# Kernel tuning notes

Hardware: AMD Instinct MI355X
Metric: run time of the kernel (lower is better)

## Reference

```python
import jax, jax.numpy as jnp
import numpy as np

B, D_IN, D_Z, D_H, D_T, D_REC = 8192, 1024, 256, 256, 16, 256


def _softplus_beta(x, beta):
    # torch F.softplus(x, beta) = (1/beta) * log(1 + exp(beta*x))
    return jax.nn.softplus(beta * x) / beta


def setup_inputs() -> dict:
    key = jax.random.key(0)
    ks = jax.random.split(key, 17)
    w = lambda k, o, i: jax.random.normal(k, (o, i), jnp.float32) * (1.0 / np.sqrt(i))
    return {
        "I_t": jax.random.uniform(ks[0], (B, D_IN), jnp.float32),
        "h_m_1": jax.random.uniform(ks[1], (B, D_H), jnp.float32),
        "z_m_1": jax.random.uniform(ks[2], (B, D_Z), jnp.float32),
        "theta_m_1": jax.random.normal(ks[3], (B, D_T), jnp.float32),
        "eps_z": jax.random.normal(ks[4], (B, D_Z), jnp.float32),
        "eps_zhat": jax.random.normal(ks[5], (B, D_Z), jnp.float32),
        "W_post_mu": w(ks[6], D_Z, D_IN),
        "W_post_lv": w(ks[7], D_Z, D_IN),
        "W_z2h": w(ks[8], D_H, D_Z),
        "W_h2h": w(ks[9], D_H, D_H),
        "W_prior_mu": w(ks[10], D_Z, D_H),
        "W_prior_lv": w(ks[11], D_Z, D_H),
        "W_i2t": w(ks[12], D_T, D_IN),
        "W_vip2t": w(ks[13], D_T, D_Z),
        "W_t2z": w(ks[14], D_Z, D_T),
        "W_rec1": w(ks[15], D_REC, D_Z),
        "W_rec2": w(ks[16], D_IN, D_REC),
    }


def reference(I_t, h_m_1, z_m_1, theta_m_1, eps_z, eps_zhat,
              W_post_mu, W_post_lv, W_z2h, W_h2h, W_prior_mu, W_prior_lv,
              W_i2t, W_vip2t, W_t2z, W_rec1, W_rec2):
    relu = jax.nn.relu
    # prior pathway (perception_only=True branch)
    mu_p = relu(h_m_1 @ W_prior_mu.T)                       # [B, D_Z]
    sigma_p = _softplus_beta(h_m_1 @ W_prior_lv.T, 1.2)     # [B, D_Z]
    # theta dynamics; vip_to_theta has Positive parametrization -> relu(W)
    theta_h = (0.5 * theta_m_1 + 0.1 * (I_t @ W_i2t.T)
               - jax.lax.stop_gradient(sigma_p) @ relu(W_vip2t).T)  # [B, D_T]
    theta = 0.001 * _softplus_beta(theta_h, 0.5)
    # posterior + reparameterized sample
    mu_q = relu(I_t @ W_post_mu.T)
    sigma_q = relu(I_t @ W_post_lv.T)
    raw_z = jnp.clip(mu_q + eps_z * sigma_q, 0.0, 1.0)
    thresholds = 10.0 * (theta @ relu(W_t2z).T)             # Positive parametrization
    z = relu(raw_z - thresholds)                            # [B, D_Z]
    # reconstruction (two bias-free linears + sigmoid)
    I_hat = jax.nn.sigmoid((z @ W_rec1.T) @ W_rec2.T)       # [B, D_IN]
    # higher-state update and prior sample
    h = relu(z_m_1 @ W_z2h.T + h_m_1 @ W_h2h.T)             # [B, D_H]
    z_hat = mu_p + eps_zhat * sigma_p                       # [B, D_Z]
    # losses (as in torch forward)
    spatial = jnp.mean((I_t - I_hat) ** 2)
    temporal = jnp.mean((jax.lax.stop_gradient(z) - z_hat) ** 2)
    energy = jnp.mean(jnp.abs(z))
    return (I_hat, z, h, z_hat, spatial, temporal, energy)
```

## Files before the change

kernel.cpp:

```cpp
#include <hip/hip_runtime.h>
#include <math.h>

#define BB 8192
#define DIN 1024
#define DZ 256
#define DH 256
#define DT 16
#define DREC 256

#define OFF_IHAT 0
#define OFF_Z    (BB * DIN)
#define OFF_H    (OFF_Z + BB * DZ)
#define OFF_ZHAT (OFF_H + BB * DH)
#define OFF_SCAL (OFF_ZHAT + BB * DZ)

#define WS_HBF   0
#define WS_ZM1   2097152
#define WS_W     4194304
#define W_PM  (WS_W + 0)
#define W_PL  (W_PM + 262144)
#define W_Z2H (W_PL + 262144)
#define W_H2H (W_Z2H + 65536)
#define W_PRM (W_H2H + 65536)
#define W_PRL (W_PRM + 65536)
#define W_I2T (W_PRL + 65536)
#define W_VIP (W_I2T + 16384)
#define W_R1  (W_VIP + 4096)
#define W_R2  (W_R1 + 65536)
#define WS_ENDW  (W_R2 + 262144)
#define WS_SIGMA WS_ENDW
#define WS_ZBF   (WS_SIGMA + 2097152)
#define WS_R1BF  (WS_ZBF + 2097152)

typedef unsigned short u16;
typedef __attribute__((ext_vector_type(8))) unsigned short u16x8;
typedef __attribute__((ext_vector_type(8))) __bf16 bf16x8;
typedef __attribute__((ext_vector_type(4))) float f32x4;

#define MFMA __builtin_amdgcn_mfma_f32_16x16x32_bf16

__device__ inline u16 f2bf(float f) {
  unsigned u = __builtin_bit_cast(unsigned, f);
  u += 0x7fff + ((u >> 16) & 1);
  return (u16)(u >> 16);
}
__device__ inline float softplus_stable(float y) {
  return (y > 20.f) ? y : log1pf(expf(y));
}
__device__ inline bf16x8 gf(const u16* p) {
  return __builtin_bit_cast(bf16x8, *(const u16x8*)p);
}
__device__ inline f32x4 fzero() { return (f32x4){0.f, 0.f, 0.f, 0.f}; }

__device__ inline float block_sum256(float v, float* rbuf) {
#pragma unroll
  for (int off = 32; off > 0; off >>= 1) v += __shfl_down(v, off, 64);
  __syncthreads();
  if ((threadIdx.x & 63) == 0) rbuf[threadIdx.x >> 6] = v;
  __syncthreads();
  return rbuf[0] + rbuf[1] + rbuf[2] + rbuf[3];
}
__device__ inline float block_sum512(float v, float* rbuf) {
#pragma unroll
  for (int off = 32; off > 0; off >>= 1) v += __shfl_down(v, off, 64);
  __syncthreads();
  if ((threadIdx.x & 63) == 0) rbuf[threadIdx.x >> 6] = v;
  __syncthreads();
  float s = 0.f;
#pragma unroll
  for (int i = 0; i < 8; ++i) s += rbuf[i];
  return s;
}

__device__ inline void decode4(int id, int rows, int& row0, int& col0) {
  int xcd = id & 7, t = id >> 3;
  col0 = (t & 3) * 64;
  row0 = ((t >> 2) * 8 + xcd) * rows;
}

__device__ inline void dmaA32(u16* tile, const u16* __restrict__ gsrc,
                              int row0, int ldk, int k0) {
  const int lane = threadIdx.x & 63, w = threadIdx.x >> 6;
  int rb = w * 8;
  int r = rb + (lane >> 3);
  int gl = (lane & 7) ^ (r & 7);
  const u16* src = gsrc + (size_t)(row0 + r) * ldk + k0 + gl * 8;
  u16* dst = tile + rb * 64;
  __builtin_amdgcn_global_load_lds(
      (const __attribute__((address_space(1))) unsigned int*)(const void*)src,
      (__attribute__((address_space(3))) unsigned int*)(void*)dst, 16, 0, 0);
}
__device__ inline void dmaB64(u16* tile, const u16* __restrict__ gsrc,
                              int row0, int ldk, int k0) {
  const int lane = threadIdx.x & 63, w = threadIdx.x >> 6;
#pragma unroll
  for (int c = 0; c < 2; ++c) {
    int rb = w * 16 + c * 8;
    int r = rb + (lane >> 3);
    int gl = (lane & 7) ^ (r & 7);
    const u16* src = gsrc + (size_t)(row0 + r) * ldk + k0 + gl * 8;
    u16* dst = tile + rb * 64;
    __builtin_amdgcn_global_load_lds(
        (const __attribute__((address_space(1))) unsigned int*)(const void*)src,
        (__attribute__((address_space(3))) unsigned int*)(void*)dst, 16, 0, 0);
  }
}
__device__ inline bf16x8 rd(const u16* tile, int r, int gl) {
  return gf(tile + r * 64 + ((gl ^ (r & 7)) * 8));
}

__device__ inline void stg64x128(u16* tile, const u16* __restrict__ g,
                                 int row0, int ldk, int k0) {
  const int lane = threadIdx.x & 63, w = threadIdx.x >> 6;
#pragma unroll
  for (int i = 0; i < 2; ++i) {
    int rb = (w * 2 + i) * 4;
    int r = rb + (lane >> 4);
    int d = lane & 15;
    int s = d ^ (r & 7);
    const u16* src = g + (size_t)(row0 + r) * ldk + k0 + s * 8;
    u16* dst = tile + rb * 128;
    __builtin_amdgcn_global_load_lds(
        (const __attribute__((address_space(1))) unsigned int*)(const void*)src,
        (__attribute__((address_space(3))) unsigned int*)(void*)dst, 16, 0, 0);
  }
}
__device__ inline void stg16x128(u16* tile, const u16* __restrict__ g,
                                 int ldk, int k0) {
  const int lane = threadIdx.x & 63, w = threadIdx.x >> 6;
  if (w < 4) {
    int rb = w * 4;
    int r = rb + (lane >> 4);
    int d = lane & 15;
    int s = d ^ (r & 7);
    const u16* src = g + (size_t)r * ldk + k0 + s * 8;
    u16* dst = tile + rb * 128;
    __builtin_amdgcn_global_load_lds(
        (const __attribute__((address_space(1))) unsigned int*)(const void*)src,
        (__attribute__((address_space(3))) unsigned int*)(void*)dst, 16, 0, 0);
  }
}
__device__ inline bf16x8 rd128(const u16* tile, int r, int j) {
  return gf(tile + r * 128 + ((j ^ (r & 7)) * 8));
}

__device__ inline void lda4(bf16x8 (&ar)[4], const u16* base, int kwin,
                            int fq) {
#pragma unroll
  for (int kk = 0; kk < 4; ++kk) ar[kk] = gf(base + kwin + kk * 32 + fq * 8);
}
__device__ inline void cmpMain(const u16* buf, bf16x8 (&ar)[4], f32x4 (&mu)[4],
                               f32x4 (&sg)[4], f32x4& tt, int frow, int fq) {
#pragma unroll
  for (int kk = 0; kk < 4; ++kk) {
    int j = kk * 4 + fq;
#pragma unroll
    for (int n = 0; n < 4; ++n) {
      mu[n] = MFMA(ar[kk], rd128(buf, n * 16 + frow, j), mu[n], 0, 0, 0);
      sg[n] = MFMA(ar[kk], rd128(buf + 8192, n * 16 + frow, j), sg[n], 0, 0, 0);
    }
    tt = MFMA(ar[kk], rd128(buf + 16384, frow, j), tt, 0, 0, 0);
  }
}
__device__ inline void cmpSig(const u16* buf, bf16x8 (&ar)[4], f32x4& tt,
                              int frow, int fq) {
#pragma unroll
  for (int kk = 0; kk < 4; ++kk)
    tt = MFMA(ar[kk], rd128(buf + 16384, frow, kk * 4 + fq), tt, 0, 0, 0);
}

__global__ __launch_bounds__(256) void k_cvt(
    const float* __restrict__ I_t, const float* __restrict__ h_m_1,
    const float* __restrict__ z_m_1, const float* __restrict__ Wpm,
    const float* __restrict__ Wpl, const float* __restrict__ Wz2h,
    const float* __restrict__ Wh2h, const float* __restrict__ Wprm,
    const float* __restrict__ Wprl, const float* __restrict__ Wi2t,
    const float* __restrict__ Wv, const float* __restrict__ Wr1,
    const float* __restrict__ Wr2, u16* __restrict__ dstI,
    u16* __restrict__ dstW) {
  const int S1 = 8388608, S2 = 10485760, S3 = 12582912, S4 = 12845056,
            S5 = 13107200, S6 = 13172736, S7 = 13238272, S8 = 13303808,
            S9 = 13369344, S10 = 13385728, S11 = 13389824, S12 = 13455360,
            S13 = 13717504;
  int nchunk = S13 / 8;
  for (int c = blockIdx.x * 256 + threadIdx.x; c < nchunk;
       c += gridDim.x * 256) {
    int f = c * 8;
    const float* src;
    float scale = 1.f;
    bool nrelu = false;
    u16* dst;
    if (f < S1) {
      src = I_t + f;
      dst = dstI + f;
    } else {
      dst = dstW + (f - S1);
      if (f < S2)       src = h_m_1 + (f - S1);
      else if (f < S3)  src = z_m_1 + (f - S2);
      else if (f < S4)  src = Wpm + (f - S3);
      else if (f < S5)  src = Wpl + (f - S4);
      else if (f < S6)  src = Wz2h + (f - S5);
      else if (f < S7)  src = Wh2h + (f - S6);
      else if (f < S8)  src = Wprm + (f - S7);
      else if (f < S9)  src = Wprl + (f - S8);
      else if (f < S10) { src = Wi2t + (f - S9);  scale = 0.1f; }
      else if (f < S11) { src = Wv + (f - S10);   nrelu = true; }
      else if (f < S12) src = Wr1 + (f - S11);
      else              src = Wr2 + (f - S12);
    }
    float4 v0 = *(const float4*)(src);
    float4 v1 = *(const float4*)(src + 4);
    float vals[8] = {v0.x, v0.y, v0.z, v0.w, v1.x, v1.y, v1.z, v1.w};
    u16x8 o;
#pragma unroll
    for (int j = 0; j < 8; ++j) {
      float x = vals[j];
      x = nrelu ? -fmaxf(x, 0.f) : x * scale;
      o[j] = f2bf(x);
    }
    *(u16x8*)(dst) = o;
  }
}

__global__ __launch_bounds__(256, 2) void k_hp(
    const u16* __restrict__ h_bf, const u16* __restrict__ zm1,
    const u16* __restrict__ Wh2h, const u16* __restrict__ Wprm,
    const u16* __restrict__ Wprl, const u16* __restrict__ Wz2h,
    const float* __restrict__ eps_zhat, float* __restrict__ h_out,
    float* __restrict__ zhat_out, u16* __restrict__ sigma_bf) {
  __shared__ __align__(16) u16 smem[2 * 14336];
  const int tid = threadIdx.x, lane = tid & 63, w = tid >> 6;
  const int frow = lane & 15, fq = lane >> 4;
  const int wr = w & 1, wc = w >> 1;
  int row0, col0;
  decode4(blockIdx.x, 32, row0, col0);

  f32x4 ah[2], am[2], as_[2];
#pragma unroll
  for (int i = 0; i < 2; ++i) { ah[i] = fzero(); am[i] = fzero(); as_[i] = fzero(); }

  dmaA32(smem, h_bf, row0, DH, 0);
  dmaB64(smem + 2048, Wh2h, col0, DH, 0);
  dmaB64(smem + 6144, Wprm, col0, DH, 0);
  dmaB64(smem + 10240, Wprl, col0, DH, 0);

#pragma unroll 1
  for (int t = 0; t < 8; ++t) {
    __syncthreads();
    u16* cs = smem + (t & 1) * 14336;
    u16* ns = smem + ((t + 1) & 1) * 14336;
    if (t < 7) {
      int u = t + 1;
      if (u < 4) {
        int k0 = u * 64;
        dmaA32(ns, h_bf, row0, DH, k0);
        dmaB64(ns + 2048, Wh2h, col0, DH, k0);
        dmaB64(ns + 6144, Wprm, col0, DH, k0);
        dmaB64(ns + 10240, Wprl, col0, DH, k0);
      } else {
        int k0 = (u - 4) * 64;
        dmaA32(ns, zm1, row0, DZ, k0);
        dmaB64(ns + 2048, Wz2h, col0, DZ, k0);
      }
    }
    const u16* As = cs;
    const u16* B0s = cs + 2048;
    if (t < 4) {
      const u16* B1s = cs + 6144;
      const u16* B2s = cs + 10240;
#pragma unroll
      for (int ks = 0; ks < 2; ++ks) {
        bf16x8 a = rd(As, wr * 16 + frow, ks * 4 + fq);
#pragma unroll
        for (int ni = 0; ni < 2; ++ni) {
          int br = wc * 32 + ni * 16 + frow;
          ah[ni]  = MFMA(a, rd(B0s, br, ks * 4 + fq), ah[ni], 0, 0, 0);
          am[ni]  = MFMA(a, rd(B1s, br, ks * 4 + fq), am[ni], 0, 0, 0);
          as_[ni] = MFMA(a, rd(B2s, br, ks * 4 + fq), as_[ni], 0, 0, 0);
        }
      }
    } else {
#pragma unroll
      for (int ks = 0; ks < 2; ++ks) {
        bf16x8 a = rd(As, wr * 16 + frow, ks * 4 + fq);
#pragma unroll
        for (int ni = 0; ni < 2; ++ni)
          ah[ni] = MFMA(a, rd(B0s, wc * 32 + ni * 16 + frow, ks * 4 + fq),
                        ah[ni], 0, 0, 0);
      }
    }
  }
  __syncthreads();
  float* ht = (float*)smem;
  float* mt = (float*)(smem + 4224);
  float* st = (float*)(smem + 8448);
#pragma unroll
  for (int ni = 0; ni < 2; ++ni)
#pragma unroll
    for (int r = 0; r < 4; ++r) {
      int lr = wr * 16 + fq * 4 + r;
      int ln = wc * 32 + ni * 16 + frow;
      ht[lr * 66 + ln] = fmaxf(ah[ni][r], 0.f);
      mt[lr * 66 + ln] = fmaxf(am[ni][r], 0.f);
      st[lr * 66 + ln] = softplus_stable(1.2f * as_[ni][r]) * (1.f / 1.2f);
    }
  __syncthreads();
  {
    int lr2 = tid >> 3, c0 = (tid & 7) * 8;
    int m2 = row0 + lr2;
    float h8[8], mu8[8], sg8[8];
#pragma unroll
    for (int j = 0; j < 8; ++j) {
      h8[j] = ht[lr2 * 66 + c0 + j];
      mu8[j] = mt[lr2 * 66 + c0 + j];
      sg8[j] = st[lr2 * 66 + c0 + j];
    }
    float* hp = h_out + (size_t)m2 * DH + col0 + c0;
    *(float4*)hp = make_float4(h8[0], h8[1], h8[2], h8[3]);
    *(float4*)(hp + 4) = make_float4(h8[4], h8[5], h8[6], h8[7]);
    const float* ep = eps_zhat + (size_t)m2 * DZ + col0 + c0;
    float4 e0 = ((const float4*)ep)[0], e1 = ((const float4*)ep)[1];
    float e8[8] = {e0.x, e0.y, e0.z, e0.w, e1.x, e1.y, e1.z, e1.w};
    float zh8[8];
    u16x8 sb;
#pragma unroll
    for (int j = 0; j < 8; ++j) {
      zh8[j] = mu8[j] + e8[j] * sg8[j];
      sb[j] = f2bf(sg8[j]);
    }
    float* zp = zhat_out + (size_t)m2 * DZ + col0 + c0;
    *(float4*)zp = make_float4(zh8[0], zh8[1], zh8[2], zh8[3]);
    *(float4*)(zp + 4) = make_float4(zh8[4], zh8[5], zh8[6], zh8[7]);
    *(u16x8*)(sigma_bf + (size_t)m2 * DZ + col0 + c0) = sb;
  }
}

__global__ __launch_bounds__(512, 2) void k_post(
    const u16* __restrict__ I_bf, const u16* __restrict__ Wpm,
    const u16* __restrict__ Wpl, const u16* __restrict__ Wi2t,
    const u16* __restrict__ Wv, const u16* __restrict__ sigma_bf,
    const float* __restrict__ theta_m_1, const float* __restrict__ W_t2z,
    const float* __restrict__ eps_z, const float* __restrict__ zhat,
    float* __restrict__ z_out, u16* __restrict__ z_bf,
    float* __restrict__ scal) {
  __shared__ __align__(16) u16 smem[2 * 18432];
  __shared__ float thwt[128 * 17 + 64 * 17];
  __shared__ float rbuf[8];
  const int tid = threadIdx.x, lane = tid & 63, w = tid >> 6;
  const int frow = lane & 15, fq = lane >> 4;
  int row0, col0;
  {
    int xcd = blockIdx.x & 7, t = blockIdx.x >> 3;
    col0 = (t & 3) * 64;
    row0 = ((t >> 2) * 8 + xcd) * 128;
  }
  u16* b0 = smem;
  u16* b1 = smem + 18432;

  f32x4 mu[4], sg[4], tt = fzero();
#pragma unroll
  for (int i = 0; i < 4; ++i) { mu[i] = fzero(); sg[i] = fzero(); }

  const u16* Abase = I_bf + (size_t)(row0 + w * 16 + frow) * DIN;
  const u16* Sbase = sigma_bf + (size_t)(row0 + w * 16 + frow) * DZ;
  bf16x8 arA[4], arB[4];

#define STGM(buf, k0)                        \
  stg64x128(buf, Wpm, col0, DIN, k0);        \
  stg64x128((buf) + 8192, Wpl, col0, DIN, k0);\
  stg16x128((buf) + 16384, Wi2t, DIN, k0)

  STGM(b0, 0);
  lda4(arA, Abase, 0, fq);
  __syncthreads(); STGM(b1, 128); lda4(arB, Abase, 128, fq);
  cmpMain(b0, arA, mu, sg, tt, frow, fq);
  __syncthreads(); STGM(b0, 256); lda4(arA, Abase, 256, fq);
  cmpMain(b1, arB, mu, sg, tt, frow, fq);
  __syncthreads(); STGM(b1, 384); lda4(arB, Abase, 384, fq);
  cmpMain(b0, arA, mu, sg, tt, frow, fq);
  __syncthreads(); STGM(b0, 512); lda4(arA, Abase, 512, fq);
  cmpMain(b1, arB, mu, sg, tt, frow, fq);
  __syncthreads(); STGM(b1, 640); lda4(arB, Abase, 640, fq);
  cmpMain(b0, arA, mu, sg, tt, frow, fq);
  __syncthreads(); STGM(b0, 768); lda4(arA, Abase, 768, fq);
  cmpMain(b1, arB, mu, sg, tt, frow, fq);
  __syncthreads(); STGM(b1, 896); lda4(arB, Abase, 896, fq);
  cmpMain(b0, arA, mu, sg, tt, frow, fq);
  __syncthreads(); stg16x128(b0 + 16384, Wv, DZ, 0); lda4(arA, Sbase, 0, fq);
  cmpMain(b1, arB, mu, sg, tt, frow, fq);
  __syncthreads(); stg16x128(b1 + 16384, Wv, DZ, 128); lda4(arB, Sbase, 128, fq);
  cmpSig(b0, arA, tt, frow, fq);
  __syncthreads();
  cmpSig(b1, arB, tt, frow, fq);
#undef STGM

  __syncthreads();
  float* mt   = (float*)smem;
  float* st   = (float*)(smem + 16896);
  float* th_s = thwt;
  float* wt_s = thwt + 128 * 17;

#pragma unroll
  for (int r = 0; r < 4; ++r) {
    int lr = w * 16 + fq * 4 + r;
    float th = 0.5f * theta_m_1[(size_t)(row0 + lr) * DT + frow] + tt[r];
    th_s[lr * 17 + frow] = 0.002f * softplus_stable(0.5f * th);
  }
  for (int idx = tid; idx < 64 * 16; idx += 512) {
    int n = idx >> 4, j = idx & 15;
    wt_s[n * 17 + j] = 10.f * fmaxf(W_t2z[(col0 + n) * DT + j], 0.f);
  }
#pragma unroll
  for (int n = 0; n < 4; ++n)
#pragma unroll
    for (int r = 0; r < 4; ++r) {
      int lr = w * 16 + fq * 4 + r;
      int ln = n * 16 + frow;
      mt[lr * 66 + ln] = fmaxf(mu[n][r], 0.f);
      st[lr * 66 + ln] = fmaxf(sg[n][r], 0.f);
    }
  __syncthreads();
  float tsum = 0.f, esum = 0.f;
  {
    int lr2 = tid >> 2, c0 = (tid & 3) * 16;
    int m2 = row0 + lr2;
    float thv[16];
#pragma unroll
    for (int j = 0; j < 16; ++j) thv[j] = th_s[lr2 * 17 + j];
#pragma unroll
    for (int gb = 0; gb < 2; ++gb) {
      int c = c0 + gb * 8;
      float mu8[8], sg8[8];
#pragma unroll
      for (int j = 0; j < 8; ++j) {
        mu8[j] = mt[lr2 * 66 + c + j];
        sg8[j] = st[lr2 * 66 + c + j];
      }
      const float* ep = eps_z + (size_t)m2 * DZ + col0 + c;
      float4 e0 = ((const float4*)ep)[0], e1 = ((const float4*)ep)[1];
      float e8[8] = {e0.x, e0.y, e0.z, e0.w, e1.x, e1.y, e1.z, e1.w};
      float z8[8];
#pragma unroll
      for (int j = 0; j < 8; ++j) {
        float raw = mu8[j] + e8[j] * sg8[j];
        raw = fminf(fmaxf(raw, 0.f), 1.f);
        float thr = 0.f;
#pragma unroll
        for (int jj = 0; jj < 16; ++jj)
          thr = fmaf(thv[jj], wt_s[(c + j) * 17 + jj], thr);
        z8[j] = fmaxf(raw - thr, 0.f);
      }
      float* zp = z_out + (size_t)m2 * DZ + col0 + c;
      *(float4*)zp = make_float4(z8[0], z8[1], z8[2], z8[3]);
      *(float4*)(zp + 4) = make_float4(z8[4], z8[5], z8[6], z8[7]);
      u16x8 zb;
#pragma unroll
      for (int j = 0; j < 8; ++j) zb[j] = f2bf(z8[j]);
      *(u16x8*)(z_bf + (size_t)m2 * DZ + col0 + c) = zb;
      const float* zhp = zhat + (size_t)m2 * DZ + col0 + c;
      float4 h0 = ((const float4*)zhp)[0], h1 = ((const float4*)zhp)[1];
      float zh8[8] = {h0.x, h0.y, h0.z, h0.w, h1.x, h1.y, h1.z, h1.w};
#pragma unroll
      for (int j = 0; j < 8; ++j) {
        float d = z8[j] - zh8[j];
        tsum += d * d;
        esum += z8[j];
      }
    }
  }
  float t = block_sum512(tsum, rbuf);
  if (tid == 0) atomicAdd(scal + 1, t * (1.f / ((float)BB * DZ)));
  float e = block_sum512(esum, rbuf);
  if (tid == 0) atomicAdd(scal + 2, e * (1.f / ((float)BB * DZ)));
}

__global__ __launch_bounds__(256, 4) void k_rec1(const u16* __restrict__ z_bf,
                                                 const u16* __restrict__ Wr1,
                                                 u16* __restrict__ r1_bf) {
  __shared__ __align__(16) u16 smem[2 * 6144];
  const int tid = threadIdx.x, lane = tid & 63, w = tid >> 6;
  const int frow = lane & 15, fq = lane >> 4;
  const int wr = w & 1, wc = w >> 1;
  int row0, col0;
  decode4(blockIdx.x, 32, row0, col0);
  f32x4 acc[2] = {fzero(), fzero()};

  dmaA32(smem, z_bf, row0, DZ, 0);
  dmaB64(smem + 2048, Wr1, col0, DZ, 0);
#pragma unroll 1
  for (int t = 0; t < 4; ++t) {
    __syncthreads();
    u16* cs = smem + (t & 1) * 6144;
    u16* ns = smem + ((t + 1) & 1) * 6144;
    if (t < 3) {
      int k0 = (t + 1) * 64;
      dmaA32(ns, z_bf, row0, DZ, k0);
      dmaB64(ns + 2048, Wr1, col0, DZ, k0);
    }
#pragma unroll
    for (int ks = 0; ks < 2; ++ks) {
      bf16x8 a = rd(cs, wr * 16 + frow, ks * 4 + fq);
#pragma unroll
      for (int ni = 0; ni < 2; ++ni)
        acc[ni] = MFMA(a, rd(cs + 2048, wc * 32 + ni * 16 + frow, ks * 4 + fq),
                       acc[ni], 0, 0, 0);
    }
  }
  __syncthreads();
  float* rt = (float*)smem;
#pragma unroll
  for (int ni = 0; ni < 2; ++ni)
#pragma unroll
    for (int r = 0; r < 4; ++r) {
      int lr = wr * 16 + fq * 4 + r;
      int ln = wc * 32 + ni * 16 + frow;
      rt[lr * 66 + ln] = acc[ni][r];
    }
  __syncthreads();
  {
    int lr2 = tid >> 3, c0 = (tid & 7) * 8;
    int m2 = row0 + lr2;
    u16x8 rb;
#pragma unroll
    for (int j = 0; j < 8; ++j) rb[j] = f2bf(rt[lr2 * 66 + c0 + j]);
    *(u16x8*)(r1_bf + (size_t)m2 * DREC + col0 + c0) = rb;
  }
}

__global__ __launch_bounds__(256, 4) void k_rec2(const u16* __restrict__ r1_bf,
                                                 const u16* __restrict__ Wr2,
                                                 const float* __restrict__ I_t,
                                                 float* __restrict__ ihat_out,
                                                 float* __restrict__ scal) {
  __shared__ __align__(16) u16 smem[2 * 8192];
  __shared__ float rbuf[4];
  const int tid = threadIdx.x, lane = tid & 63, w = tid >> 6;
  const int frow = lane & 15, fq = lane >> 4;
  int row0, col0;
  {
    int id = blockIdx.x;
    int xcd = id & 7, t = id >> 3;
    col0 = (t & 15) * 64;
    row0 = ((t >> 4) * 8 + xcd) * 64;
  }
  f32x4 acc[4] = {fzero(), fzero(), fzero(), fzero()};

  dmaB64(smem, r1_bf, row0, DREC, 0);
  dmaB64(smem + 4096, Wr2, col0, DREC, 0);
#pragma unroll 1
  for (int t = 0; t < 4; ++t) {
    __syncthreads();
    u16* cs = smem + (t & 1) * 8192;
    u16* ns = smem + ((t + 1) & 1) * 8192;
    if (t < 3) {
      int k0 = (t + 1) * 64;
      dmaB64(ns, r1_bf, row0, DREC, k0);
      dmaB64(ns + 4096, Wr2, col0, DREC, k0);
    }
#pragma unroll
    for (int ks = 0; ks < 2; ++ks) {
      bf16x8 a = rd(cs, w * 16 + frow, ks * 4 + fq);
#pragma unroll
      for (int ni = 0; ni < 4; ++ni)
        acc[ni] = MFMA(a, rd(cs + 4096, ni * 16 + frow, ks * 4 + fq),
                       acc[ni], 0, 0, 0);
    }
  }
  float lsum = 0.f;
  float* it = (float*)smem;
#pragma unroll 1
  for (int p = 0; p < 2; ++p) {
    __syncthreads();
    if ((w >> 1) == p) {
#pragma unroll
      for (int ni = 0; ni < 4; ++ni)
#pragma unroll
        for (int r = 0; r < 4; ++r) {
          int lrl = (w & 1) * 16 + fq * 4 + r;
          int ln = ni * 16 + frow;
          it[lrl * 66 + ln] = 1.f / (1.f + expf(-acc[ni][r]));
        }
    }
    __syncthreads();
    int lr2 = tid >> 3, c0 = (tid & 7) * 8;
    int m2 = row0 + p * 32 + lr2;
    float i8[8];
#pragma unroll
    for (int j = 0; j < 8; ++j) i8[j] = it[lr2 * 66 + c0 + j];
    float* op = ihat_out + (size_t)m2 * DIN + col0 + c0;
    *(float4*)op = make_float4(i8[0], i8[1], i8[2], i8[3]);
    *(float4*)(op + 4) = make_float4(i8[4], i8[5], i8[6], i8[7]);
    const float* ip = I_t + (size_t)m2 * DIN + col0 + c0;
    float4 a0 = ((const float4*)ip)[0], a1 = ((const float4*)ip)[1];
    float t8[8] = {a0.x, a0.y, a0.z, a0.w, a1.x, a1.y, a1.z, a1.w};
#pragma unroll
    for (int j = 0; j < 8; ++j) {
      float d = t8[j] - i8[j];
      lsum += d * d;
    }
  }
  float s = block_sum256(lsum, rbuf);
  if (tid == 0) atomicAdd(scal + 0, s * (1.f / ((float)BB * DIN)));
}

extern "C" void kernel_launch(void* const* d_in, const int* in_sizes, int n_in,
                              void* d_out, int out_size, void* d_ws,
                              size_t ws_size, hipStream_t stream) {
  const float* I_t       = (const float*)d_in[0];
  const float* h_m_1     = (const float*)d_in[1];
  const float* z_m_1     = (const float*)d_in[2];
  const float* theta_m_1 = (const float*)d_in[3];
  const float* eps_z     = (const float*)d_in[4];
  const float* eps_zhat  = (const float*)d_in[5];
  const float* W_post_mu = (const float*)d_in[6];
  const float* W_post_lv = (const float*)d_in[7];
  const float* W_z2h     = (const float*)d_in[8];
  const float* W_h2h     = (const float*)d_in[9];
  const float* W_prior_mu= (const float*)d_in[10];
  const float* W_prior_lv= (const float*)d_in[11];
  const float* W_i2t     = (const float*)d_in[12];
  const float* W_vip2t   = (const float*)d_in[13];
  const float* W_t2z     = (const float*)d_in[14];
  const float* W_rec1    = (const float*)d_in[15];
  const float* W_rec2    = (const float*)d_in[16];

  float* out = (float*)d_out;
  float* ihat = out + OFF_IHAT;
  float* zout = out + OFF_Z;
  float* hout = out + OFF_H;
  float* zhat = out + OFF_ZHAT;
  float* scal = out + OFF_SCAL;

  u16* ws_u = (u16*)d_ws;
  u16* I_bf = (u16*)ihat;
  u16* h_bf = ws_u + WS_HBF;
  u16* zm1_bf = ws_u + WS_ZM1;
  u16* sigma_bf = ws_u + WS_SIGMA;
  u16* z_bf = ws_u + WS_ZBF;
  u16* r1_bf = ws_u + WS_R1BF;

  hipMemsetAsync(scal, 0, 3 * sizeof(float), stream);

  k_cvt<<<2048, 256, 0, stream>>>(I_t, h_m_1, z_m_1, W_post_mu, W_post_lv,
                                  W_z2h, W_h2h, W_prior_mu, W_prior_lv, W_i2t,
                                  W_vip2t, W_rec1, W_rec2, I_bf, ws_u + WS_HBF);

  k_hp<<<1024, 256, 0, stream>>>(h_bf, zm1_bf, ws_u + W_H2H, ws_u + W_PRM,
                                 ws_u + W_PRL, ws_u + W_Z2H, eps_zhat, hout,
                                 zhat, sigma_bf);
  k_post<<<256, 512, 0, stream>>>(I_bf, ws_u + W_PM, ws_u + W_PL,
                                  ws_u + W_I2T, ws_u + W_VIP, sigma_bf,
                                  theta_m_1, W_t2z, eps_z, zhat, zout, z_bf,
                                  scal);
  k_rec1<<<1024, 256, 0, stream>>>(z_bf, ws_u + W_R1, r1_bf);
  k_rec2<<<2048, 256, 0, stream>>>(r1_bf, ws_u + W_R2, I_t, ihat, scal);
}
```

Before: 236.3 us.

## Retile k_hp as 128x64 register-A kernel; single-buffer rec1/rec2 LDS

k_hp is rewritten in the k_post style. It uses 512-thread blocks covering 128 rows by 64 columns, loads the A operands (h, z_m_1) straight into registers, and double-buffers the weight tiles in LDS with 128-wide K steps. This cuts the block count from 1024 to 256 and is meant to raise MFMA work per block and weight reuse. Separately, k_rec1 and k_rec2 drop their double buffering for a single LDS buffer with two barriers per K step, which saves shared memory but serializes load and compute.

```diff
diff --git a/kernel.cpp b/kernel.cpp
--- a/kernel.cpp
+++ b/kernel.cpp
@@ -167,6 +167,30 @@
 #pragma unroll
   for (int kk = 0; kk < 4; ++kk)
     tt = MFMA(ar[kk], rd128(buf + 16384, frow, kk * 4 + fq), tt, 0, 0, 0);
+}
+__device__ inline void hpCmp3(const u16* buf, bf16x8 (&ar)[4], f32x4 (&ah)[4],
+                              f32x4 (&am)[4], f32x4 (&as_)[4], int frow,
+                              int fq) {
+#pragma unroll
+  for (int kk = 0; kk < 4; ++kk) {
+    int j = kk * 4 + fq;
+#pragma unroll
+    for (int n = 0; n < 4; ++n) {
+      ah[n]  = MFMA(ar[kk], rd128(buf, n * 16 + frow, j), ah[n], 0, 0, 0);
+      am[n]  = MFMA(ar[kk], rd128(buf + 8192, n * 16 + frow, j), am[n], 0, 0, 0);
+      as_[n] = MFMA(ar[kk], rd128(buf + 16384, n * 16 + frow, j), as_[n], 0, 0, 0);
+    }
+  }
+}
+__device__ inline void hpCmp1(const u16* buf, bf16x8 (&ar)[4], f32x4 (&ah)[4],
+                              int frow, int fq) {
+#pragma unroll
+  for (int kk = 0; kk < 4; ++kk) {
+    int j = kk * 4 + fq;
+#pragma unroll
+    for (int n = 0; n < 4; ++n)
+      ah[n] = MFMA(ar[kk], rd128(buf, n * 16 + frow, j), ah[n], 0, 0, 0);
+  }
 }
 
 __global__ __launch_bounds__(256) void k_cvt(
@@ -222,92 +246,74 @@
   }
 }
 
-__global__ __launch_bounds__(256, 2) void k_hp(
+__global__ __launch_bounds__(512, 2) void k_hp(
     const u16* __restrict__ h_bf, const u16* __restrict__ zm1,
     const u16* __restrict__ Wh2h, const u16* __restrict__ Wprm,
     const u16* __restrict__ Wprl, const u16* __restrict__ Wz2h,
     const float* __restrict__ eps_zhat, float* __restrict__ h_out,
     float* __restrict__ zhat_out, u16* __restrict__ sigma_bf) {
-  __shared__ __align__(16) u16 smem[2 * 14336];
+  __shared__ __align__(16) u16 smem[2 * 24576];
   const int tid = threadIdx.x, lane = tid & 63, w = tid >> 6;
   const int frow = lane & 15, fq = lane >> 4;
-  const int wr = w & 1, wc = w >> 1;
   int row0, col0;
-  decode4(blockIdx.x, 32, row0, col0);
-
-  f32x4 ah[2], am[2], as_[2];
-#pragma unroll
-  for (int i = 0; i < 2; ++i) { ah[i] = fzero(); am[i] = fzero(); as_[i] = fzero(); }
-
-  dmaA32(smem, h_bf, row0, DH, 0);
-  dmaB64(smem + 2048, Wh2h, col0, DH, 0);
-  dmaB64(smem + 6144, Wprm, col0, DH, 0);
-  dmaB64(smem + 10240, Wprl, col0, DH, 0);
-
+  {
+    int xcd = blockIdx.x & 7, t = blockIdx.x >> 3;
+    col0 = (t & 3) * 64;
+    row0 = ((t >> 2) * 8 + xcd) * 128;
+  }
+  u16* b0 = smem;
+  u16* b1 = smem + 24576;
+
+  f32x4 ah[4], am[4], as_[4];
+#pragma unroll
+  for (int n = 0; n < 4; ++n) { ah[n] = fzero(); am[n] = fzero(); as_[n] = fzero(); }
+
+  const u16* Ah = h_bf + (size_t)(row0 + w * 16 + frow) * DH;
+  const u16* Az = zm1 + (size_t)(row0 + w * 16 + frow) * DZ;
+  bf16x8 arA[4], arB[4];
+
+  stg64x128(b0, Wh2h, col0, DH, 0);
+  stg64x128(b0 + 8192, Wprm, col0, DH, 0);
+  stg64x128(b0 + 16384, Wprl, col0, DH, 0);
+  lda4(arA, Ah, 0, fq);
+  __syncthreads();
+  stg64x128(b1, Wh2h, col0, DH, 128);
+  stg64x128(b1 + 8192, Wprm, col0, DH, 128);
+  stg64x128(b1 + 16384, Wprl, col0, DH, 128);
+  lda4(arB, Ah, 128, fq);
+  hpCmp3(b0, arA, ah, am, as_, frow, fq);
+  __syncthreads();
+  stg64x128(b0, Wz2h, col0, DZ, 0);
+  lda4(arA, Az, 0, fq);
+  hpCmp3(b1, arB, ah, am, as_, frow, fq);
+  __syncthreads();
+  stg64x128(b1, Wz2h, col0, DZ, 128);
+  lda4(arB, Az, 128, fq);
+  hpCmp1(b0, arA, ah, frow, fq);
+  __syncthreads();
+  hpCmp1(b1, arB, ah, frow, fq);
+
+  float* ht = (float*)smem;
+  float* mt = (float*)(smem + 8448);
+  float* st = (float*)(smem + 16896);
 #pragma unroll 1
-  for (int t = 0; t < 8; ++t) {
-    __syncthreads();
-    u16* cs = smem + (t & 1) * 14336;
-    u16* ns = smem + ((t + 1) & 1) * 14336;
-    if (t < 7) {
-      int u = t + 1;
-      if (u < 4) {
-        int k0 = u * 64;
-        dmaA32(ns, h_bf, row0, DH, k0);
-        dmaB64(ns + 2048, Wh2h, col0, DH, k0);
-        dmaB64(ns + 6144, Wprm, col0, DH, k0);
-        dmaB64(ns + 10240, Wprl, col0, DH, k0);
-      } else {
-        int k0 = (u - 4) * 64;
-        dmaA32(ns, zm1, row0, DZ, k0);
-        dmaB64(ns + 2048, Wz2h, col0, DZ, k0);
-      }
-    }
-    const u16* As = cs;
-    const u16* B0s = cs + 2048;
-    if (t < 4) {
-      const u16* B1s = cs + 6144;
-      const u16* B2s = cs + 10240;
-#pragma unroll
-      for (int ks = 0; ks < 2; ++ks) {
-        bf16x8 a = rd(As, wr * 16 + frow, ks * 4 + fq);
-#pragma unroll
-        for (int ni = 0; ni < 2; ++ni) {
-          int br = wc * 32 + ni * 16 + frow;
-          ah[ni]  = MFMA(a, rd(B0s, br, ks * 4 + fq), ah[ni], 0, 0, 0);
-          am[ni]  = MFMA(a, rd(B1s, br, ks * 4 + fq), am[ni], 0, 0, 0);
-          as_[ni] = MFMA(a, rd(B2s, br, ks * 4 + fq), as_[ni], 0, 0, 0);
+  for (int p = 0; p < 2; ++p) {
+    __syncthreads();
+    if ((w >> 2) == p) {
+#pragma unroll
+      for (int n = 0; n < 4; ++n)
+#pragma unroll
+        for (int r = 0; r < 4; ++r) {
+          int lrl = (w & 3) * 16 + fq * 4 + r;
+          int ln = n * 16 + frow;
+          ht[lrl * 66 + ln] = fmaxf(ah[n][r], 0.f);
+          mt[lrl * 66 + ln] = fmaxf(am[n][r], 0.f);
+          st[lrl * 66 + ln] = softplus_stable(1.2f * as_[n][r]) * (1.f / 1.2f);
         }
-      }
-    } else {
-#pragma unroll
-      for (int ks = 0; ks < 2; ++ks) {
-        bf16x8 a = rd(As, wr * 16 + frow, ks * 4 + fq);
-#pragma unroll
-        for (int ni = 0; ni < 2; ++ni)
-          ah[ni] = MFMA(a, rd(B0s, wc * 32 + ni * 16 + frow, ks * 4 + fq),
-                        ah[ni], 0, 0, 0);
-      }
-    }
-  }
-  __syncthreads();
-  float* ht = (float*)smem;
-  float* mt = (float*)(smem + 4224);
-  float* st = (float*)(smem + 8448);
-#pragma unroll
-  for (int ni = 0; ni < 2; ++ni)
-#pragma unroll
-    for (int r = 0; r < 4; ++r) {
-      int lr = wr * 16 + fq * 4 + r;
-      int ln = wc * 32 + ni * 16 + frow;
-      ht[lr * 66 + ln] = fmaxf(ah[ni][r], 0.f);
-      mt[lr * 66 + ln] = fmaxf(am[ni][r], 0.f);
-      st[lr * 66 + ln] = softplus_stable(1.2f * as_[ni][r]) * (1.f / 1.2f);
-    }
-  __syncthreads();
-  {
+    }
+    __syncthreads();
     int lr2 = tid >> 3, c0 = (tid & 7) * 8;
-    int m2 = row0 + lr2;
+    int m2 = row0 + p * 64 + lr2;
     float h8[8], mu8[8], sg8[8];
 #pragma unroll
     for (int j = 0; j < 8; ++j) {
@@ -365,9 +371,9 @@
   const u16* Sbase = sigma_bf + (size_t)(row0 + w * 16 + frow) * DZ;
   bf16x8 arA[4], arB[4];
 
-#define STGM(buf, k0)                        \
-  stg64x128(buf, Wpm, col0, DIN, k0);        \
-  stg64x128((buf) + 8192, Wpl, col0, DIN, k0);\
+#define STGM(buf, k0)                           \
+  stg64x128(buf, Wpm, col0, DIN, k0);           \
+  stg64x128((buf) + 8192, Wpl, col0, DIN, k0);  \
   stg16x128((buf) + 16384, Wi2t, DIN, k0)
 
   STGM(b0, 0);
@@ -477,32 +483,26 @@
 __global__ __launch_bounds__(256, 4) void k_rec1(const u16* __restrict__ z_bf,
                                                  const u16* __restrict__ Wr1,
                                                  u16* __restrict__ r1_bf) {
-  __shared__ __align__(16) u16 smem[2 * 6144];
+  __shared__ __align__(16) u16 smem[2048 + 4096];
+  u16* As = smem;
+  u16* B0s = smem + 2048;
   const int tid = threadIdx.x, lane = tid & 63, w = tid >> 6;
   const int frow = lane & 15, fq = lane >> 4;
   const int wr = w & 1, wc = w >> 1;
   int row0, col0;
   decode4(blockIdx.x, 32, row0, col0);
   f32x4 acc[2] = {fzero(), fzero()};
-
-  dmaA32(smem, z_bf, row0, DZ, 0);
-  dmaB64(smem + 2048, Wr1, col0, DZ, 0);
-#pragma unroll 1
-  for (int t = 0; t < 4; ++t) {
-    __syncthreads();
-    u16* cs = smem + (t & 1) * 6144;
-    u16* ns = smem + ((t + 1) & 1) * 6144;
-    if (t < 3) {
-      int k0 = (t + 1) * 64;
-      dmaA32(ns, z_bf, row0, DZ, k0);
-      dmaB64(ns + 2048, Wr1, col0, DZ, k0);
-    }
+  for (int k0 = 0; k0 < DZ; k0 += 64) {
+    __syncthreads();
+    dmaA32(As, z_bf, row0, DZ, k0);
+    dmaB64(B0s, Wr1, col0, DZ, k0);
+    __syncthreads();
 #pragma unroll
     for (int ks = 0; ks < 2; ++ks) {
-      bf16x8 a = rd(cs, wr * 16 + frow, ks * 4 + fq);
+      bf16x8 a = rd(As, wr * 16 + frow, ks * 4 + fq);
 #pragma unroll
       for (int ni = 0; ni < 2; ++ni)
-        acc[ni] = MFMA(a, rd(cs + 2048, wc * 32 + ni * 16 + frow, ks * 4 + fq),
+        acc[ni] = MFMA(a, rd(B0s, wc * 32 + ni * 16 + frow, ks * 4 + fq),
                        acc[ni], 0, 0, 0);
     }
   }
@@ -532,7 +532,9 @@
                                                  const float* __restrict__ I_t,
                                                  float* __restrict__ ihat_out,
                                                  float* __restrict__ scal) {
-  __shared__ __align__(16) u16 smem[2 * 8192];
+  __shared__ __align__(16) u16 smem[4096 + 4096];
+  u16* As = smem;
+  u16* B0s = smem + 4096;
   __shared__ float rbuf[4];
   const int tid = threadIdx.x, lane = tid & 63, w = tid >> 6;
   const int frow = lane & 15, fq = lane >> 4;
@@ -544,26 +546,17 @@
     row0 = ((t >> 4) * 8 + xcd) * 64;
   }
   f32x4 acc[4] = {fzero(), fzero(), fzero(), fzero()};
-
-  dmaB64(smem, r1_bf, row0, DREC, 0);
-  dmaB64(smem + 4096, Wr2, col0, DREC, 0);
-#pragma unroll 1
-  for (int t = 0; t < 4; ++t) {
-    __syncthreads();
-    u16* cs = smem + (t & 1) * 8192;
-    u16* ns = smem + ((t + 1) & 1) * 8192;
-    if (t < 3) {
-      int k0 = (t + 1) * 64;
-      dmaB64(ns, r1_bf, row0, DREC, k0);
-      dmaB64(ns + 4096, Wr2, col0, DREC, k0);
-    }
+  for (int k0 = 0; k0 < DREC; k0 += 64) {
+    __syncthreads();
+    dmaB64(As, r1_bf, row0, DREC, k0);
+    dmaB64(B0s, Wr2, col0, DREC, k0);
+    __syncthreads();
 #pragma unroll
     for (int ks = 0; ks < 2; ++ks) {
-      bf16x8 a = rd(cs, w * 16 + frow, ks * 4 + fq);
+      bf16x8 a = rd(As, w * 16 + frow, ks * 4 + fq);
 #pragma unroll
       for (int ni = 0; ni < 4; ++ni)
-        acc[ni] = MFMA(a, rd(cs + 4096, ni * 16 + frow, ks * 4 + fq),
-                       acc[ni], 0, 0, 0);
+        acc[ni] = MFMA(a, rd(B0s, ni * 16 + frow, ks * 4 + fq), acc[ni], 0, 0, 0);
     }
   }
   float lsum = 0.f;
@@ -645,9 +638,9 @@
                                   W_z2h, W_h2h, W_prior_mu, W_prior_lv, W_i2t,
                                   W_vip2t, W_rec1, W_rec2, I_bf, ws_u + WS_HBF);
 
-  k_hp<<<1024, 256, 0, stream>>>(h_bf, zm1_bf, ws_u + W_H2H, ws_u + W_PRM,
-                                 ws_u + W_PRL, ws_u + W_Z2H, eps_zhat, hout,
-                                 zhat, sigma_bf);
+  k_hp<<<256, 512, 0, stream>>>(h_bf, zm1_bf, ws_u + W_H2H, ws_u + W_PRM,
+                                ws_u + W_PRL, ws_u + W_Z2H, eps_zhat, hout,
+                                zhat, sigma_bf);
   k_post<<<256, 512, 0, stream>>>(I_bf, ws_u + W_PM, ws_u + W_PL,
                                   ws_u + W_I2T, ws_u + W_VIP, sigma_bf,
                                   theta_m_1, W_t2z, eps_z, zhat, zout, z_bf,
```

New measurement: 236.9 us. No clear change (+0.2%).
